# Kernel optimization log

Hardware: AMD Instinct MI355X
Metric: run time of the kernel (lower is better)

## Reference

```python
import jax, jax.numpy as jnp
import numpy as np


def _kabsch_rmsd(p, c):
    # p, c: [N, 3]
    pm = jnp.mean(p, axis=0)  # [3]
    cm = jnp.mean(c, axis=0)  # [3]
    # 3x3 cross-covariance
    A = (p - pm).T @ (c - cm)
    U, S, Vt = jnp.linalg.svd(A, full_matrices=False)
    d = jnp.sign(jnp.linalg.det(A))
    # corr_mat = diag([1, 1, d]);  rotation = U @ corr_mat @ Vt
    scale = jnp.concatenate([jnp.ones((2,), dtype=p.dtype), d[None].astype(p.dtype)])
    R = U @ (scale[:, None] * Vt)  # [3,3]
    # translation = pm - R @ cm; aligned coords = (R @ c^T)^T + translation
    aligned = c @ R.T + (pm - R @ cm)
    sq = jnp.sum((p - aligned) ** 2, axis=1)  # [N]
    return jnp.sqrt(jnp.mean(sq))


def setup_inputs() -> dict:
    key = jax.random.key(0)
    k1, k2 = jax.random.split(key)
    B, N = 4096, 2048
    coords_pred = jax.random.normal(k1, (B, N, 3), dtype=jnp.float32)
    coords = jax.random.normal(k2, (B, N, 3), dtype=jnp.float32)
    return {"coords_pred": coords_pred, "coords": coords}


def reference(coords_pred, coords):
    # Batched Kabsch alignment + RMSD; default mode='global', return_all=False
    # -> mean over the per-sample RMSDs.
    rmsds = jax.vmap(_kabsch_rmsd)(coords_pred, coords)  # [B]
    return jnp.mean(rmsds)
```

## Files before the change

kernel.cpp:

```cpp
#include <hip/hip_runtime.h>
#include <math.h>

#define NPTS 2048
#define BLOCK 256

__global__ __launch_bounds__(BLOCK) void kabsch_kernel(
    const float* __restrict__ P, const float* __restrict__ C,
    float* __restrict__ out, int B) {
  const int b = blockIdx.x;
  const int t = threadIdx.x;
  const float4* p4 = (const float4*)(P + (size_t)b * (NPTS * 3));
  const float4* c4 = (const float4*)(C + (size_t)b * (NPTS * 3));

  float acc[17];
#pragma unroll
  for (int i = 0; i < 17; i++) acc[i] = 0.f;

#pragma unroll
  for (int k = 0; k < (NPTS * 3 / 4) / (BLOCK * 3); k++) {
    const int base = k * (BLOCK * 3) + 3 * t;
    const float4 pa = p4[base], pb = p4[base + 1], pq = p4[base + 2];
    const float4 ca = c4[base], cb = c4[base + 1], cq = c4[base + 2];
    const float Px[4] = {pa.x, pa.w, pb.z, pq.y};
    const float Py[4] = {pa.y, pb.x, pb.w, pq.z};
    const float Pz[4] = {pa.z, pb.y, pq.x, pq.w};
    const float Cx[4] = {ca.x, ca.w, cb.z, cq.y};
    const float Cy[4] = {ca.y, cb.x, cb.w, cq.z};
    const float Cz[4] = {ca.z, cb.y, cq.x, cq.w};
#pragma unroll
    for (int i = 0; i < 4; i++) {
      const float px = Px[i], py = Py[i], pz = Pz[i];
      const float cx = Cx[i], cy = Cy[i], cz = Cz[i];
      acc[0] += px; acc[1] += py; acc[2] += pz;
      acc[3] += cx; acc[4] += cy; acc[5] += cz;
      acc[6] += px * px + py * py + pz * pz;
      acc[7] += cx * cx + cy * cy + cz * cz;
      acc[8]  += px * cx; acc[9]  += px * cy; acc[10] += px * cz;
      acc[11] += py * cx; acc[12] += py * cy; acc[13] += py * cz;
      acc[14] += pz * cx; acc[15] += pz * cy; acc[16] += pz * cz;
    }
  }

#pragma unroll
  for (int off = 32; off > 0; off >>= 1) {
#pragma unroll
    for (int i = 0; i < 17; i++) acc[i] += __shfl_down(acc[i], off);
  }
  __shared__ float red[BLOCK / 64][17];
  const int wave = t >> 6, lane = t & 63;
  if (lane == 0) {
#pragma unroll
    for (int i = 0; i < 17; i++) red[wave][i] = acc[i];
  }
  __syncthreads();

  if (t == 0) {
    double s[17];
#pragma unroll
    for (int i = 0; i < 17; i++) {
      float v = red[0][i];
      for (int w = 1; w < BLOCK / 64; w++) v += red[w][i];
      s[i] = (double)v;
    }
    const double invN = 1.0 / (double)NPTS;
    const double spx = s[0], spy = s[1], spz = s[2];
    const double scx = s[3], scy = s[4], scz = s[5];
    const double Ep = s[6] - (spx * spx + spy * spy + spz * spz) * invN;
    const double Ec = s[7] - (scx * scx + scy * scy + scz * scz) * invN;
    const double a00 = s[8]  - spx * scx * invN, a01 = s[9]  - spx * scy * invN, a02 = s[10] - spx * scz * invN;
    const double a10 = s[11] - spy * scx * invN, a11 = s[12] - spy * scy * invN, a12 = s[13] - spy * scz * invN;
    const double a20 = s[14] - spz * scx * invN, a21 = s[15] - spz * scy * invN, a22 = s[16] - spz * scz * invN;
    const double det = a00 * (a11 * a22 - a12 * a21)
                     - a01 * (a10 * a22 - a12 * a20)
                     + a02 * (a10 * a21 - a11 * a20);
    const double b00 = a00 * a00 + a10 * a10 + a20 * a20;
    const double b11 = a01 * a01 + a11 * a11 + a21 * a21;
    const double b22 = a02 * a02 + a12 * a12 + a22 * a22;
    const double b01 = a00 * a01 + a10 * a11 + a20 * a21;
    const double b02 = a00 * a02 + a10 * a12 + a20 * a22;
    const double b12 = a01 * a02 + a11 * a12 + a21 * a22;
    const double q = (b00 + b11 + b22) / 3.0;
    const double p1 = b01 * b01 + b02 * b02 + b12 * b12;
    const double d0 = b00 - q, d1 = b11 - q, d2 = b22 - q;
    const double p2 = d0 * d0 + d1 * d1 + d2 * d2 + 2.0 * p1;
    double e1, e2, e3;
    if (p2 < 1e-30) {
      e1 = e2 = e3 = q;
    } else {
      const double pp = sqrt(p2 / 6.0);
      const double inv = 1.0 / pp;
      const double c00 = d0 * inv, c11 = d1 * inv, c22 = d2 * inv;
      const double c01 = b01 * inv, c02 = b02 * inv, c12 = b12 * inv;
      double r = 0.5 * (c00 * (c11 * c22 - c12 * c12)
                      - c01 * (c01 * c22 - c12 * c02)
                      + c02 * (c01 * c12 - c11 * c02));
      r = fmin(1.0, fmax(-1.0, r));
      const double phi = acos(r) / 3.0;
      e1 = q + 2.0 * pp * cos(phi);
      e3 = q + 2.0 * pp * cos(phi + 2.0943951023931953);
      e2 = 3.0 * q - e1 - e3;
    }
    const double s1 = sqrt(fmax(e1, 0.0));
    const double s2 = sqrt(fmax(e2, 0.0));
    const double s3 = sqrt(fmax(e3, 0.0));
    const double dsign = (det > 0.0) ? 1.0 : ((det < 0.0) ? -1.0 : 0.0);
    const double trRS = s1 + s2 + dsign * s3;
    const double msd = (Ep + Ec - 2.0 * trRS) * invN;
    const double rmsd = sqrt(fmax(msd, 0.0));
    atomicAdd(out, (float)(rmsd / (double)B));
  }
}

extern "C" void kernel_launch(void* const* d_in, const int* in_sizes, int n_in,
                              void* d_out, int out_size, void* d_ws, size_t ws_size,
                              hipStream_t stream) {
  const float* P = (const float*)d_in[0];
  const float* C = (const float*)d_in[1];
  float* out = (float*)d_out;
  const int B = in_sizes[0] / (NPTS * 3);
  hipMemsetAsync(out, 0, sizeof(float), stream);
  kabsch_kernel<<<B, BLOCK, 0, stream>>>(P, C, out, B);
}
```

Before: 215.8 us.

## Assign one batch sample per wavefront with software-prefetched loads

Each 64-lane wavefront now processes a whole sample, four samples per block, so the per-sample reduction needs only wave shuffles and no shared-memory cross-wave step. The loop over 8 chunks double-buffers the float4 loads, prefetching the next chunk before computing the current one, and launch bounds request higher occupancy. Atomics drop fourfold because each block adds one combined value. The serial double-precision eigen solve now runs on lane 0 of every wave, and the prefetch raises register use.

```diff
diff --git a/kernel.cpp b/kernel.cpp
--- a/kernel.cpp
+++ b/kernel.cpp
@@ -3,111 +3,123 @@
 
 #define NPTS 2048
 #define BLOCK 256
+#define BPB 4
+#define CHUNKS (NPTS / (64 * 4))
 
-__global__ __launch_bounds__(BLOCK) void kabsch_kernel(
+__global__ __launch_bounds__(BLOCK, 4) void kabsch_kernel(
     const float* __restrict__ P, const float* __restrict__ C,
     float* __restrict__ out, int B) {
-  const int b = blockIdx.x;
-  const int t = threadIdx.x;
-  const float4* p4 = (const float4*)(P + (size_t)b * (NPTS * 3));
-  const float4* c4 = (const float4*)(C + (size_t)b * (NPTS * 3));
+  const int wave = threadIdx.x >> 6;
+  const int lane = threadIdx.x & 63;
+  const int b = blockIdx.x * BPB + wave;
 
-  float acc[17];
+  double rmsd = 0.0;
+  if (b < B) {
+    const float4* p4 = (const float4*)(P + (size_t)b * (NPTS * 3));
+    const float4* c4 = (const float4*)(C + (size_t)b * (NPTS * 3));
+
+    float acc[17];
 #pragma unroll
-  for (int i = 0; i < 17; i++) acc[i] = 0.f;
+    for (int i = 0; i < 17; i++) acc[i] = 0.f;
+
+    int base = 3 * lane;
+    float4 pa = p4[base], pb = p4[base + 1], pq = p4[base + 2];
+    float4 ca = c4[base], cb = c4[base + 1], cq = c4[base + 2];
+#pragma unroll
+    for (int k = 0; k < CHUNKS; k++) {
+      float4 npa, npb, npq, nca, ncb, ncq;
+      if (k + 1 < CHUNKS) {
+        const int nb = base + 64 * 3;
+        npa = p4[nb]; npb = p4[nb + 1]; npq = p4[nb + 2];
+        nca = c4[nb]; ncb = c4[nb + 1]; ncq = c4[nb + 2];
+        base = nb;
+      }
+      const float Px[4] = {pa.x, pa.w, pb.z, pq.y};
+      const float Py[4] = {pa.y, pb.x, pb.w, pq.z};
+      const float Pz[4] = {pa.z, pb.y, pq.x, pq.w};
+      const float Cx[4] = {ca.x, ca.w, cb.z, cq.y};
+      const float Cy[4] = {ca.y, cb.x, cb.w, cq.z};
+      const float Cz[4] = {ca.z, cb.y, cq.x, cq.w};
+#pragma unroll
+      for (int i = 0; i < 4; i++) {
+        const float px = Px[i], py = Py[i], pz = Pz[i];
+        const float cx = Cx[i], cy = Cy[i], cz = Cz[i];
+        acc[0] += px; acc[1] += py; acc[2] += pz;
+        acc[3] += cx; acc[4] += cy; acc[5] += cz;
+        acc[6] += px * px + py * py + pz * pz;
+        acc[7] += cx * cx + cy * cy + cz * cz;
+        acc[8]  += px * cx; acc[9]  += px * cy; acc[10] += px * cz;
+        acc[11] += py * cx; acc[12] += py * cy; acc[13] += py * cz;
+        acc[14] += pz * cx; acc[15] += pz * cy; acc[16] += pz * cz;
+      }
+      pa = npa; pb = npb; pq = npq;
+      ca = nca; cb = ncb; cq = ncq;
+    }
 
 #pragma unroll
-  for (int k = 0; k < (NPTS * 3 / 4) / (BLOCK * 3); k++) {
-    const int base = k * (BLOCK * 3) + 3 * t;
-    const float4 pa = p4[base], pb = p4[base + 1], pq = p4[base + 2];
-    const float4 ca = c4[base], cb = c4[base + 1], cq = c4[base + 2];
-    const float Px[4] = {pa.x, pa.w, pb.z, pq.y};
-    const float Py[4] = {pa.y, pb.x, pb.w, pq.z};
-    const float Pz[4] = {pa.z, pb.y, pq.x, pq.w};
-    const float Cx[4] = {ca.x, ca.w, cb.z, cq.y};
-    const float Cy[4] = {ca.y, cb.x, cb.w, cq.z};
-    const float Cz[4] = {ca.z, cb.y, cq.x, cq.w};
+    for (int off = 32; off > 0; off >>= 1) {
 #pragma unroll
-    for (int i = 0; i < 4; i++) {
-      const float px = Px[i], py = Py[i], pz = Pz[i];
-      const float cx = Cx[i], cy = Cy[i], cz = Cz[i];
-      acc[0] += px; acc[1] += py; acc[2] += pz;
-      acc[3] += cx; acc[4] += cy; acc[5] += cz;
-      acc[6] += px * px + py * py + pz * pz;
-      acc[7] += cx * cx + cy * cy + cz * cz;
-      acc[8]  += px * cx; acc[9]  += px * cy; acc[10] += px * cz;
-      acc[11] += py * cx; acc[12] += py * cy; acc[13] += py * cz;
-      acc[14] += pz * cx; acc[15] += pz * cy; acc[16] += pz * cz;
+      for (int i = 0; i < 17; i++) acc[i] += __shfl_down(acc[i], off);
+    }
+
+    if (lane == 0) {
+      double s[17];
+#pragma unroll
+      for (int i = 0; i < 17; i++) s[i] = (double)acc[i];
+      const double invN = 1.0 / (double)NPTS;
+      const double spx = s[0], spy = s[1], spz = s[2];
+      const double scx = s[3], scy = s[4], scz = s[5];
+      const double Ep = s[6] - (spx * spx + spy * spy + spz * spz) * invN;
+      const double Ec = s[7] - (scx * scx + scy * scy + scz * scz) * invN;
+      const double a00 = s[8]  - spx * scx * invN, a01 = s[9]  - spx * scy * invN, a02 = s[10] - spx * scz * invN;
+      const double a10 = s[11] - spy * scx * invN, a11 = s[12] - spy * scy * invN, a12 = s[13] - spy * scz * invN;
+      const double a20 = s[14] - spz * scx * invN, a21 = s[15] - spz * scy * invN, a22 = s[16] - spz * scz * invN;
+      const double det = a00 * (a11 * a22 - a12 * a21)
+                       - a01 * (a10 * a22 - a12 * a20)
+                       + a02 * (a10 * a21 - a11 * a20);
+      const double b00 = a00 * a00 + a10 * a10 + a20 * a20;
+      const double b11 = a01 * a01 + a11 * a11 + a21 * a21;
+      const double b22 = a02 * a02 + a12 * a12 + a22 * a22;
+      const double b01 = a00 * a01 + a10 * a11 + a20 * a21;
+      const double b02 = a00 * a02 + a10 * a12 + a20 * a22;
+      const double b12 = a01 * a02 + a11 * a12 + a21 * a22;
+      const double q = (b00 + b11 + b22) / 3.0;
+      const double p1 = b01 * b01 + b02 * b02 + b12 * b12;
+      const double d0 = b00 - q, d1 = b11 - q, d2 = b22 - q;
+      const double p2 = d0 * d0 + d1 * d1 + d2 * d2 + 2.0 * p1;
+      double e1, e2, e3;
+      if (p2 < 1e-30) {
+        e1 = e2 = e3 = q;
+      } else {
+        const double pp = sqrt(p2 / 6.0);
+        const double inv = 1.0 / pp;
+        const double c00 = d0 * inv, c11 = d1 * inv, c22 = d2 * inv;
+        const double c01 = b01 * inv, c02 = b02 * inv, c12 = b12 * inv;
+        double r = 0.5 * (c00 * (c11 * c22 - c12 * c12)
+                        - c01 * (c01 * c22 - c12 * c02)
+                        + c02 * (c01 * c12 - c11 * c02));
+        r = fmin(1.0, fmax(-1.0, r));
+        const double phi = acos(r) / 3.0;
+        e1 = q + 2.0 * pp * cos(phi);
+        e3 = q + 2.0 * pp * cos(phi + 2.0943951023931953);
+        e2 = 3.0 * q - e1 - e3;
+      }
+      const double s1 = sqrt(fmax(e1, 0.0));
+      const double s2 = sqrt(fmax(e2, 0.0));
+      const double s3 = sqrt(fmax(e3, 0.0));
+      const double dsign = (det > 0.0) ? 1.0 : ((det < 0.0) ? -1.0 : 0.0);
+      const double trRS = s1 + s2 + dsign * s3;
+      const double msd = (Ep + Ec - 2.0 * trRS) * invN;
+      rmsd = sqrt(fmax(msd, 0.0));
     }
   }
 
-#pragma unroll
-  for (int off = 32; off > 0; off >>= 1) {
-#pragma unroll
-    for (int i = 0; i < 17; i++) acc[i] += __shfl_down(acc[i], off);
-  }
-  __shared__ float red[BLOCK / 64][17];
-  const int wave = t >> 6, lane = t & 63;
-  if (lane == 0) {
-#pragma unroll
-    for (int i = 0; i < 17; i++) red[wave][i] = acc[i];
-  }
+  __shared__ double red[BPB];
+  if (lane == 0) red[wave] = rmsd;
   __syncthreads();
-
-  if (t == 0) {
-    double s[17];
-#pragma unroll
-    for (int i = 0; i < 17; i++) {
-      float v = red[0][i];
-      for (int w = 1; w < BLOCK / 64; w++) v += red[w][i];
-      s[i] = (double)v;
-    }
-    const double invN = 1.0 / (double)NPTS;
-    const double spx = s[0], spy = s[1], spz = s[2];
-    const double scx = s[3], scy = s[4], scz = s[5];
-    const double Ep = s[6] - (spx * spx + spy * spy + spz * spz) * invN;
-    const double Ec = s[7] - (scx * scx + scy * scy + scz * scz) * invN;
-    const double a00 = s[8]  - spx * scx * invN, a01 = s[9]  - spx * scy * invN, a02 = s[10] - spx * scz * invN;
-    const double a10 = s[11] - spy * scx * invN, a11 = s[12] - spy * scy * invN, a12 = s[13] - spy * scz * invN;
-    const double a20 = s[14] - spz * scx * invN, a21 = s[15] - spz * scy * invN, a22 = s[16] - spz * scz * invN;
-    const double det = a00 * (a11 * a22 - a12 * a21)
-                     - a01 * (a10 * a22 - a12 * a20)
-                     + a02 * (a10 * a21 - a11 * a20);
-    const double b00 = a00 * a00 + a10 * a10 + a20 * a20;
-    const double b11 = a01 * a01 + a11 * a11 + a21 * a21;
-    const double b22 = a02 * a02 + a12 * a12 + a22 * a22;
-    const double b01 = a00 * a01 + a10 * a11 + a20 * a21;
-    const double b02 = a00 * a02 + a10 * a12 + a20 * a22;
-    const double b12 = a01 * a02 + a11 * a12 + a21 * a22;
-    const double q = (b00 + b11 + b22) / 3.0;
-    const double p1 = b01 * b01 + b02 * b02 + b12 * b12;
-    const double d0 = b00 - q, d1 = b11 - q, d2 = b22 - q;
-    const double p2 = d0 * d0 + d1 * d1 + d2 * d2 + 2.0 * p1;
-    double e1, e2, e3;
-    if (p2 < 1e-30) {
-      e1 = e2 = e3 = q;
-    } else {
-      const double pp = sqrt(p2 / 6.0);
-      const double inv = 1.0 / pp;
-      const double c00 = d0 * inv, c11 = d1 * inv, c22 = d2 * inv;
-      const double c01 = b01 * inv, c02 = b02 * inv, c12 = b12 * inv;
-      double r = 0.5 * (c00 * (c11 * c22 - c12 * c12)
-                      - c01 * (c01 * c22 - c12 * c02)
-                      + c02 * (c01 * c12 - c11 * c02));
-      r = fmin(1.0, fmax(-1.0, r));
-      const double phi = acos(r) / 3.0;
-      e1 = q + 2.0 * pp * cos(phi);
-      e3 = q + 2.0 * pp * cos(phi + 2.0943951023931953);
-      e2 = 3.0 * q - e1 - e3;
-    }
-    const double s1 = sqrt(fmax(e1, 0.0));
-    const double s2 = sqrt(fmax(e2, 0.0));
-    const double s3 = sqrt(fmax(e3, 0.0));
-    const double dsign = (det > 0.0) ? 1.0 : ((det < 0.0) ? -1.0 : 0.0);
-    const double trRS = s1 + s2 + dsign * s3;
-    const double msd = (Ep + Ec - 2.0 * trRS) * invN;
-    const double rmsd = sqrt(fmax(msd, 0.0));
-    atomicAdd(out, (float)(rmsd / (double)B));
+  if (threadIdx.x == 0) {
+    const double sum = red[0] + red[1] + red[2] + red[3];
+    atomicAdd(out, (float)(sum / (double)B));
   }
 }
 
@@ -119,5 +131,5 @@
   float* out = (float*)d_out;
   const int B = in_sizes[0] / (NPTS * 3);
   hipMemsetAsync(out, 0, sizeof(float), stream);
-  kabsch_kernel<<<B, BLOCK, 0, stream>>>(P, C, out, B);
+  kabsch_kernel<<<(B + BPB - 1) / BPB, BLOCK, 0, stream>>>(P, C, out, B);
 }
```

New measurement: 218.0 us. No clear change (+1.0%).
